# Kernel tuning notes

Measured on AMD Instinct MI355X. Metric: run time of the kernel, lower is better.

## Reference

```python
import jax, jax.numpy as jnp
import numpy as np

N_NODES = 100000
N_EDGES = 1000000
D = 64


def _sage_conv(x_src, x_self, src, dst, W_self, W_neigh, b, n_nodes):
    # mean aggregation over in-neighbors: gather src feats, segment-sum into dst
    gathered = x_src[src]                                            # [E, D]
    summed = jax.ops.segment_sum(gathered, dst, num_segments=n_nodes)  # [N, D]
    deg = jax.ops.segment_sum(jnp.ones_like(dst, dtype=x_src.dtype), dst,
                              num_segments=n_nodes)                  # [N]
    mean = summed / jnp.maximum(deg, 1.0)[:, None]  # zero-degree -> 0 (DGL semantics)
    # DGL SAGEConv: fc_self (with bias) + fc_neigh (no bias)
    return x_self @ W_self + b + mean @ W_neigh


def setup_inputs() -> dict:
    key = jax.random.key(0)
    ks = jax.random.split(key, 8)
    s = 1.0 / np.sqrt(D)
    return {
        "x": jax.random.normal(ks[0], (N_NODES, D), dtype=jnp.float32),
        "src": jax.random.randint(ks[1], (N_EDGES,), 0, N_NODES, dtype=jnp.int32),
        "dst": jax.random.randint(ks[2], (N_EDGES,), 0, N_NODES, dtype=jnp.int32),
        "W_self1": jax.random.normal(ks[3], (D, D), dtype=jnp.float32) * s,
        "W_neigh1": jax.random.normal(ks[4], (D, D), dtype=jnp.float32) * s,
        "b1": jnp.zeros((D,), dtype=jnp.float32),
        "W_self2": jax.random.normal(ks[5], (D, D), dtype=jnp.float32) * s,
        "W_neigh2": jax.random.normal(ks[6], (D, D), dtype=jnp.float32) * s,
        "b2": jnp.zeros((D,), dtype=jnp.float32),
    }


def reference(x, src, dst, W_self1, W_neigh1, b1, W_self2, W_neigh2, b2):
    n = x.shape[0]
    h = _sage_conv(x, x, src, dst, W_self1, W_neigh1, b1, n)
    h = jax.nn.relu(h)
    out = _sage_conv(h, h, src, dst, W_self2, W_neigh2, b2, n)
    return out
```

## Files before the change

kernel.cpp:

```cpp
#include <hip/hip_runtime.h>

#define DFEAT 64
typedef unsigned short bf16_t;

typedef __bf16 bf16x8 __attribute__((ext_vector_type(8)));
typedef float f32x4 __attribute__((ext_vector_type(4)));

#define NPB_SHIFT 7
#define NPB 128
#define BCAP 2048
#define ATILE 8192
#define MEAN_STRIDE 72

__device__ __forceinline__ float bf2f(unsigned short u) {
    union { unsigned int i; float f; } v;
    v.i = ((unsigned int)u) << 16;
    return v.f;
}
__device__ __forceinline__ float bflo(unsigned int u) {
    union { unsigned int i; float f; } v;
    v.i = u << 16;
    return v.f;
}
__device__ __forceinline__ float bfhi(unsigned int u) {
    union { unsigned int i; float f; } v;
    v.i = u & 0xFFFF0000u;
    return v.f;
}
__device__ __forceinline__ unsigned short f2bf(float f) {
    unsigned int u = __float_as_uint(f);
    u += 0x7FFFu + ((u >> 16) & 1u);
    return (unsigned short)(u >> 16);
}

__global__ __launch_bounds__(256) void prep_all(const int* __restrict__ src,
                                                const int* __restrict__ dst,
                                                int* __restrict__ gcur,
                                                int* __restrict__ packbuf,
                                                int n_edges, int nbuck,
                                                const float* __restrict__ x,
                                                bf16_t* __restrict__ xb, int n_half,
                                                const float* __restrict__ Ws1,
                                                const float* __restrict__ Wn1,
                                                const float* __restrict__ Ws2,
                                                const float* __restrict__ Wn2,
                                                bf16_t* __restrict__ wf1,
                                                bf16_t* __restrict__ wf2,
                                                int ab, int cb) {
    const int tid = threadIdx.x;
    const int blk = blockIdx.x;
    if (blk < ab) {
        __shared__ int hist[1024];
        __shared__ int cur[1024];
        const long ebase = (long)blk * ATILE;
        for (int i = tid; i < nbuck; i += 256) hist[i] = 0;
        __syncthreads();
        for (int i = 0; i < ATILE / 256; ++i) {
            long e = ebase + i * 256 + tid;
            if (e < n_edges) atomicAdd(&hist[dst[e] >> NPB_SHIFT], 1);
        }
        __syncthreads();
        for (int b = tid; b < nbuck; b += 256) {
            int h = hist[b];
            cur[b] = h ? atomicAdd(&gcur[b], h) : 0;
        }
        __syncthreads();
        for (int i = 0; i < ATILE / 256; ++i) {
            long e = ebase + i * 256 + tid;
            if (e < n_edges) {
                int d = dst[e];
                int b = d >> NPB_SHIFT;
                int slot = atomicAdd(&cur[b], 1);
                if (slot < BCAP)
                    packbuf[(size_t)b * BCAP + slot] = ((d & (NPB - 1)) << 17) | src[e];
            }
        }
    } else if (blk < ab + cb) {
        int t = (blk - ab) * 256 + tid;
        if (t < n_half) {
            float2 v = ((const float2*)x)[t];
            ushort2 o;
            o.x = f2bf(v.x);
            o.y = f2bf(v.y);
            ((ushort2*)xb)[t] = o;
        }
    } else {
        for (int i = tid; i < 16 * 64 * 8; i += 256) {
            int j = i & 7;
            int l = (i >> 3) & 63;
            int f = i >> 9;
            int kk = f >> 2, nt = f & 3;
            int k = kk * 32 + (l >> 4) * 8 + j;
            int col = nt * 16 + (l & 15);
            float v1 = (k < 64) ? Ws1[k * 64 + col] : Wn1[(k - 64) * 64 + col];
            float v2 = (k < 64) ? Ws2[k * 64 + col] : Wn2[(k - 64) * 64 + col];
            wf1[i] = f2bf(v1);
            wf2[i] = f2bf(v2);
        }
    }
}

__global__ __launch_bounds__(256) void fused_layer(const bf16_t* __restrict__ featb,
                                                   const int* __restrict__ gcur,
                                                   const int* __restrict__ packbuf,
                                                   const bf16_t* __restrict__ wf,
                                                   const float* __restrict__ bias,
                                                   float* __restrict__ outf,
                                                   bf16_t* __restrict__ outb,
                                                   int n_nodes, int do_relu) {
    __shared__ int    elist[BCAP];
    __shared__ bf16_t meanL[NPB * MEAN_STRIDE];
    __shared__ int    hist[NPB];
    __shared__ int    scanb[NPB];
    __shared__ int    cur[NPB];

    const int tid = threadIdx.x;
    const int b   = blockIdx.x;

    if (tid < NPB) hist[tid] = 0;
    __syncthreads();

    const int count = min(gcur[b], BCAP);
    const int* pb = packbuf + (size_t)b * BCAP;

    int pkreg[BCAP / 256];
#pragma unroll
    for (int k = 0; k < BCAP / 256; ++k) {
        int i = tid + k * 256;
        if (i < count) {
            int pk = pb[i];
            pkreg[k] = pk;
            atomicAdd(&hist[(pk >> 17) & (NPB - 1)], 1);
        }
    }
    __syncthreads();

    int hv = (tid < NPB) ? hist[tid] : 0;
    if (tid < NPB) scanb[tid] = hv;
    __syncthreads();
    for (int off = 1; off < NPB; off <<= 1) {
        int t = 0;
        if (tid < NPB && tid >= off) t = scanb[tid - off];
        __syncthreads();
        if (tid < NPB) scanb[tid] += t;
        __syncthreads();
    }
    if (tid < NPB) {
        int ex = scanb[tid] - hv;
        scanb[tid] = ex;
        cur[tid]   = ex;
    }
    __syncthreads();

#pragma unroll
    for (int k = 0; k < BCAP / 256; ++k) {
        int i = tid + k * 256;
        if (i < count) {
            int pk = pkreg[k];
            int dl = (pk >> 17) & (NPB - 1);
            int pos = atomicAdd(&cur[dl], 1);
            elist[pos] = pk & 0x1FFFF;
        }
    }
    __syncthreads();

    const int oct = tid >> 3;
    const int lo  = tid & 7;
#pragma unroll
    for (int n = 0; n < 4; ++n) {
        int r  = oct * 4 + n;
        int s0 = scanb[r];
        int c  = hist[r];
        float s0f = 0.f, s1f = 0.f, s2f = 0.f, s3f = 0.f;
        float s4f = 0.f, s5f = 0.f, s6f = 0.f, s7f = 0.f;
        int i = 0;
        for (; i + 4 <= c; i += 4) {
            int e0 = elist[s0 + i + 0];
            int e1 = elist[s0 + i + 1];
            int e2 = elist[s0 + i + 2];
            int e3 = elist[s0 + i + 3];
            uint4 u0 = *(const uint4*)(featb + (size_t)e0 * DFEAT + lo * 8);
            uint4 u1 = *(const uint4*)(featb + (size_t)e1 * DFEAT + lo * 8);
            uint4 u2 = *(const uint4*)(featb + (size_t)e2 * DFEAT + lo * 8);
            uint4 u3 = *(const uint4*)(featb + (size_t)e3 * DFEAT + lo * 8);
            s0f += bflo(u0.x) + bflo(u1.x) + bflo(u2.x) + bflo(u3.x);
            s1f += bfhi(u0.x) + bfhi(u1.x) + bfhi(u2.x) + bfhi(u3.x);
            s2f += bflo(u0.y) + bflo(u1.y) + bflo(u2.y) + bflo(u3.y);
            s3f += bfhi(u0.y) + bfhi(u1.y) + bfhi(u2.y) + bfhi(u3.y);
            s4f += bflo(u0.z) + bflo(u1.z) + bflo(u2.z) + bflo(u3.z);
            s5f += bfhi(u0.z) + bfhi(u1.z) + bfhi(u2.z) + bfhi(u3.z);
            s6f += bflo(u0.w) + bflo(u1.w) + bflo(u2.w) + bflo(u3.w);
            s7f += bfhi(u0.w) + bfhi(u1.w) + bfhi(u2.w) + bfhi(u3.w);
        }
        for (; i < c; ++i) {
            int e0 = elist[s0 + i];
            uint4 u = *(const uint4*)(featb + (size_t)e0 * DFEAT + lo * 8);
            s0f += bflo(u.x); s1f += bfhi(u.x);
            s2f += bflo(u.y); s3f += bfhi(u.y);
            s4f += bflo(u.z); s5f += bfhi(u.z);
            s6f += bflo(u.w); s7f += bfhi(u.w);
        }
        float inv = (c > 0) ? 1.0f / (float)c : 0.0f;
        uint4 o;
        o.x = (unsigned int)f2bf(s0f * inv) | ((unsigned int)f2bf(s1f * inv) << 16);
        o.y = (unsigned int)f2bf(s2f * inv) | ((unsigned int)f2bf(s3f * inv) << 16);
        o.z = (unsigned int)f2bf(s4f * inv) | ((unsigned int)f2bf(s5f * inv) << 16);
        o.w = (unsigned int)f2bf(s6f * inv) | ((unsigned int)f2bf(s7f * inv) << 16);
        *(uint4*)(meanL + (size_t)r * MEAN_STRIDE + lo * 8) = o;
    }
    __syncthreads();

    const int lane = tid & 63;
    const int wave = tid >> 6;
    const int q    = lane >> 4;
    const int cgl  = lane & 15;
    const int nodeBase = b << NPB_SHIFT;

    bf16x8 a[2][4];
#pragma unroll
    for (int slab = 0; slab < 2; ++slab) {
        const int r = wave * 32 + slab * 16 + cgl;
        int nodeA = nodeBase + r;
        if (nodeA >= n_nodes) nodeA = n_nodes - 1;
        const bf16_t* xrow = featb + (size_t)nodeA * DFEAT + q * 8;
        a[slab][0] = *(const bf16x8*)(xrow);
        a[slab][1] = *(const bf16x8*)(xrow + 32);
        const bf16_t* mrow = meanL + (size_t)r * MEAN_STRIDE + q * 8;
        a[slab][2] = *(const bf16x8*)(mrow);
        a[slab][3] = *(const bf16x8*)(mrow + 32);
    }

    f32x4 acc[2][4] = {};
#pragma unroll
    for (int nt = 0; nt < 4; ++nt) {
        bf16x8 bf[4];
#pragma unroll
        for (int kk = 0; kk < 4; ++kk)
            bf[kk] = *(const bf16x8*)(wf + (size_t)((kk * 4 + nt) * 64 + lane) * 8);
#pragma unroll
        for (int slab = 0; slab < 2; ++slab) {
#pragma unroll
            for (int kk = 0; kk < 4; ++kk)
                acc[slab][nt] = __builtin_amdgcn_mfma_f32_16x16x32_bf16(
                    a[slab][kk], bf[kk], acc[slab][nt], 0, 0, 0);
        }
    }

#pragma unroll
    for (int slab = 0; slab < 2; ++slab) {
#pragma unroll
        for (int nt = 0; nt < 4; ++nt) {
            const float bl = bias[nt * 16 + cgl];
#pragma unroll
            for (int reg = 0; reg < 4; ++reg) {
                int node = nodeBase + wave * 32 + slab * 16 + q * 4 + reg;
                if (node >= n_nodes) continue;
                float v = acc[slab][nt][reg] + bl;
                if (do_relu) v = fmaxf(v, 0.0f);
                if (outf) outf[(size_t)node * DFEAT + nt * 16 + cgl] = v;
                else      outb[(size_t)node * DFEAT + nt * 16 + cgl] = f2bf(v);
            }
        }
    }
}


extern "C" void kernel_launch(void* const* d_in, const int* in_sizes, int n_in,
                              void* d_out, int out_size, void* d_ws, size_t ws_size,
                              hipStream_t stream) {
    const float* x       = (const float*)d_in[0];
    const int*   src     = (const int*)d_in[1];
    const int*   dst     = (const int*)d_in[2];
    const float* Wself1  = (const float*)d_in[3];
    const float* Wneigh1 = (const float*)d_in[4];
    const float* b1      = (const float*)d_in[5];
    const float* Wself2  = (const float*)d_in[6];
    const float* Wneigh2 = (const float*)d_in[7];
    const float* b2      = (const float*)d_in[8];
    float* out = (float*)d_out;

    const int n_nodes = in_sizes[0] / DFEAT;
    const int n_edges = in_sizes[1];
    const int nbuck   = (n_nodes + NPB - 1) >> NPB_SHIFT;

    int* gcur       = (int*)d_ws;
    bf16_t* wf1     = (bf16_t*)(gcur + 1024);
    bf16_t* wf2     = wf1 + 16 * 64 * 8;
    int* packbuf    = (int*)(wf2 + 16 * 64 * 8);
    bf16_t* xb      = (bf16_t*)(packbuf + (size_t)nbuck * BCAP);
    bf16_t* hb      = xb + (size_t)n_nodes * DFEAT;

    const int n_half = n_nodes * DFEAT / 2;
    const int cb = (n_half + 255) / 256;
    const int ab = (n_edges + ATILE - 1) / ATILE;

    hipMemsetAsync(gcur, 0, 1024 * sizeof(int), stream);
    prep_all<<<ab + cb + 1, 256, 0, stream>>>(src, dst, gcur, packbuf, n_edges, nbuck,
                                              x, xb, n_half,
                                              Wself1, Wneigh1, Wself2, Wneigh2,
                                              wf1, wf2, ab, cb);

    fused_layer<<<nbuck, 256, 0, stream>>>(xb, gcur, packbuf, wf1, b1,
                                           nullptr, hb, n_nodes, 1);
    fused_layer<<<nbuck, 256, 0, stream>>>(hb, gcur, packbuf, wf2, b2,
                                           out, nullptr, n_nodes, 0);
}
```

Baseline: 186.7 us.

## Merge prep and both SAGE layers into one cooperative persistent kernel

Replaces the memset plus three kernel launches with a single cooperative kernel of 768 persistent blocks. Grid-wide syncs separate the cast/weight prep, edge bucketing, layer 1 and layer 2, and each block loops over buckets. Edge slices shrink from 8192 to 2048 edges, and the histogram scratch reuses the meanL shared buffer. The aim is to remove launch gaps and tail effects, at the cost of grid-sync overhead and a fixed grid that handles 782 buckets in roughly one and a bit waves. A fallback path runs the old multi-kernel scheme if the cooperative launch fails.

```diff
diff --git a/kernel.cpp b/kernel.cpp
--- a/kernel.cpp
+++ b/kernel.cpp
@@ -1,4 +1,7 @@
 #include <hip/hip_runtime.h>
+#include <hip/hip_cooperative_groups.h>
+
+namespace cg = cooperative_groups;
 
 #define DFEAT 64
 typedef unsigned short bf16_t;
@@ -9,14 +12,10 @@
 #define NPB_SHIFT 7
 #define NPB 128
 #define BCAP 2048
-#define ATILE 8192
+#define ESLICE 2048
 #define MEAN_STRIDE 72
-
-__device__ __forceinline__ float bf2f(unsigned short u) {
-    union { unsigned int i; float f; } v;
-    v.i = ((unsigned int)u) << 16;
-    return v.f;
-}
+#define COOP_GRID 768
+
 __device__ __forceinline__ float bflo(unsigned int u) {
     union { unsigned int i; float f; } v;
     v.i = u << 16;
@@ -33,96 +32,74 @@
     return (unsigned short)(u >> 16);
 }
 
-__global__ __launch_bounds__(256) void prep_all(const int* __restrict__ src,
-                                                const int* __restrict__ dst,
-                                                int* __restrict__ gcur,
-                                                int* __restrict__ packbuf,
-                                                int n_edges, int nbuck,
-                                                const float* __restrict__ x,
-                                                bf16_t* __restrict__ xb, int n_half,
-                                                const float* __restrict__ Ws1,
-                                                const float* __restrict__ Wn1,
-                                                const float* __restrict__ Ws2,
-                                                const float* __restrict__ Wn2,
-                                                bf16_t* __restrict__ wf1,
-                                                bf16_t* __restrict__ wf2,
-                                                int ab, int cb) {
+
+__device__ __forceinline__ void cast_range(const float* __restrict__ x,
+                                           bf16_t* __restrict__ xb, int lo, int hi) {
+    for (int t = lo + threadIdx.x; t < hi; t += 256) {
+        float2 v = ((const float2*)x)[t];
+        ushort2 o;
+        o.x = f2bf(v.x);
+        o.y = f2bf(v.y);
+        ((ushort2*)xb)[t] = o;
+    }
+}
+
+__device__ __forceinline__ void prep_w_dev(const float* __restrict__ Ws1,
+                                           const float* __restrict__ Wn1,
+                                           const float* __restrict__ Ws2,
+                                           const float* __restrict__ Wn2,
+                                           bf16_t* __restrict__ wf1,
+                                           bf16_t* __restrict__ wf2) {
+    for (int i = threadIdx.x; i < 16 * 64 * 8; i += 256) {
+        int j = i & 7;
+        int l = (i >> 3) & 63;
+        int f = i >> 9;
+        int kk = f >> 2, nt = f & 3;
+        int k = kk * 32 + (l >> 4) * 8 + j;
+        int col = nt * 16 + (l & 15);
+        float v1 = (k < 64) ? Ws1[k * 64 + col] : Wn1[(k - 64) * 64 + col];
+        float v2 = (k < 64) ? Ws2[k * 64 + col] : Wn2[(k - 64) * 64 + col];
+        wf1[i] = f2bf(v1);
+        wf2[i] = f2bf(v2);
+    }
+}
+
+__device__ __forceinline__ void bucket_slice(const int* __restrict__ src,
+                                             const int* __restrict__ dst,
+                                             int* __restrict__ gcur,
+                                             int* __restrict__ packbuf,
+                                             int n_edges, int nbuck, long ebase,
+                                             int* bhist, int* bcur) {
     const int tid = threadIdx.x;
-    const int blk = blockIdx.x;
-    if (blk < ab) {
-        __shared__ int hist[1024];
-        __shared__ int cur[1024];
-        const long ebase = (long)blk * ATILE;
-        for (int i = tid; i < nbuck; i += 256) hist[i] = 0;
-        __syncthreads();
-        for (int i = 0; i < ATILE / 256; ++i) {
-            long e = ebase + i * 256 + tid;
-            if (e < n_edges) atomicAdd(&hist[dst[e] >> NPB_SHIFT], 1);
-        }
-        __syncthreads();
-        for (int b = tid; b < nbuck; b += 256) {
-            int h = hist[b];
-            cur[b] = h ? atomicAdd(&gcur[b], h) : 0;
-        }
-        __syncthreads();
-        for (int i = 0; i < ATILE / 256; ++i) {
-            long e = ebase + i * 256 + tid;
-            if (e < n_edges) {
-                int d = dst[e];
-                int b = d >> NPB_SHIFT;
-                int slot = atomicAdd(&cur[b], 1);
-                if (slot < BCAP)
-                    packbuf[(size_t)b * BCAP + slot] = ((d & (NPB - 1)) << 17) | src[e];
-            }
-        }
-    } else if (blk < ab + cb) {
-        int t = (blk - ab) * 256 + tid;
-        if (t < n_half) {
-            float2 v = ((const float2*)x)[t];
-            ushort2 o;
-            o.x = f2bf(v.x);
-            o.y = f2bf(v.y);
-            ((ushort2*)xb)[t] = o;
-        }
-    } else {
-        for (int i = tid; i < 16 * 64 * 8; i += 256) {
-            int j = i & 7;
-            int l = (i >> 3) & 63;
-            int f = i >> 9;
-            int kk = f >> 2, nt = f & 3;
-            int k = kk * 32 + (l >> 4) * 8 + j;
-            int col = nt * 16 + (l & 15);
-            float v1 = (k < 64) ? Ws1[k * 64 + col] : Wn1[(k - 64) * 64 + col];
-            float v2 = (k < 64) ? Ws2[k * 64 + col] : Wn2[(k - 64) * 64 + col];
-            wf1[i] = f2bf(v1);
-            wf2[i] = f2bf(v2);
-        }
-    }
-}
-
-__global__ __launch_bounds__(256) void fused_layer(const bf16_t* __restrict__ featb,
-                                                   const int* __restrict__ gcur,
-                                                   const int* __restrict__ packbuf,
-                                                   const bf16_t* __restrict__ wf,
-                                                   const float* __restrict__ bias,
-                                                   float* __restrict__ outf,
-                                                   bf16_t* __restrict__ outb,
-                                                   int n_nodes, int do_relu) {
-    __shared__ int    elist[BCAP];
-    __shared__ bf16_t meanL[NPB * MEAN_STRIDE];
-    __shared__ int    hist[NPB];
-    __shared__ int    scanb[NPB];
-    __shared__ int    cur[NPB];
-
+    for (int i = tid; i < 1024; i += 256) bhist[i] = 0;
+    __syncthreads();
+    for (int i = 0; i < ESLICE / 256; ++i) {
+        long e = ebase + i * 256 + tid;
+        if (e < n_edges) atomicAdd(&bhist[dst[e] >> NPB_SHIFT], 1);
+    }
+    __syncthreads();
+    for (int bb = tid; bb < nbuck; bb += 256) {
+        int h = bhist[bb];
+        bcur[bb] = h ? atomicAdd(&gcur[bb], h) : 0;
+    }
+    __syncthreads();
+    for (int i = 0; i < ESLICE / 256; ++i) {
+        long e = ebase + i * 256 + tid;
+        if (e < n_edges) {
+            int d = dst[e];
+            int bb = d >> NPB_SHIFT;
+            int slot = atomicAdd(&bcur[bb], 1);
+            if (slot < BCAP)
+                packbuf[(size_t)bb * BCAP + slot] = ((d & (NPB - 1)) << 17) | src[e];
+        }
+    }
+}
+
+__device__ __forceinline__ void build_sort(const int* __restrict__ pb, int count,
+                                           int* elist, int* hist, int* scanb, int* curL) {
     const int tid = threadIdx.x;
-    const int b   = blockIdx.x;
-
     if (tid < NPB) hist[tid] = 0;
     __syncthreads();
-
-    const int count = min(gcur[b], BCAP);
-    const int* pb = packbuf + (size_t)b * BCAP;
-
     int pkreg[BCAP / 256];
 #pragma unroll
     for (int k = 0; k < BCAP / 256; ++k) {
@@ -134,7 +111,6 @@
         }
     }
     __syncthreads();
-
     int hv = (tid < NPB) ? hist[tid] : 0;
     if (tid < NPB) scanb[tid] = hv;
     __syncthreads();
@@ -148,21 +124,31 @@
     if (tid < NPB) {
         int ex = scanb[tid] - hv;
         scanb[tid] = ex;
-        cur[tid]   = ex;
-    }
-    __syncthreads();
-
+        curL[tid]  = ex;
+    }
+    __syncthreads();
 #pragma unroll
     for (int k = 0; k < BCAP / 256; ++k) {
         int i = tid + k * 256;
         if (i < count) {
             int pk = pkreg[k];
             int dl = (pk >> 17) & (NPB - 1);
-            int pos = atomicAdd(&cur[dl], 1);
+            int pos = atomicAdd(&curL[dl], 1);
             elist[pos] = pk & 0x1FFFF;
         }
     }
     __syncthreads();
+}
+
+__device__ __forceinline__ void layer_body(const bf16_t* __restrict__ featb,
+                                           const bf16_t* __restrict__ wf,
+                                           const float* __restrict__ bias,
+                                           float* __restrict__ outf,
+                                           bf16_t* __restrict__ outb,
+                                           int n_nodes, int do_relu, int b,
+                                           int* elist, bf16_t* meanL,
+                                           int* hist, int* scanb) {
+    const int tid = threadIdx.x;
 
     const int oct = tid >> 3;
     const int lo  = tid & 7;
@@ -264,6 +250,114 @@
     }
 }
 
+__global__ __launch_bounds__(256, 3) void sage_all(
+        const int* __restrict__ src, const int* __restrict__ dst,
+        const float* __restrict__ x,
+        const float* __restrict__ Ws1, const float* __restrict__ Wn1,
+        const float* __restrict__ bias1,
+        const float* __restrict__ Ws2, const float* __restrict__ Wn2,
+        const float* __restrict__ bias2,
+        float* __restrict__ out,
+        int* __restrict__ gcur, bf16_t* __restrict__ wf1, bf16_t* __restrict__ wf2,
+        int* __restrict__ packbuf, bf16_t* __restrict__ xb, bf16_t* __restrict__ hb,
+        int n_nodes, int n_edges, int n_half, int nbuck) {
+    __shared__ int    elist[BCAP];
+    __shared__ bf16_t meanL[NPB * MEAN_STRIDE];
+    __shared__ int    hist[NPB];
+    __shared__ int    scanb[NPB];
+    __shared__ int    curL[NPB];
+
+    cg::grid_group grid = cg::this_grid();
+    const int tid  = threadIdx.x;
+    const int blk  = blockIdx.x;
+    const int nblk = gridDim.x;
+
+    if (blk == 0)
+        for (int i = tid; i < 1024; i += 256) gcur[i] = 0;
+    {
+        int per = (n_half + nblk - 1) / nblk;
+        int lo  = blk * per;
+        int hi  = min(lo + per, n_half);
+        cast_range(x, xb, lo, hi);
+    }
+    if (blk == nblk - 1)
+        prep_w_dev(Ws1, Wn1, Ws2, Wn2, wf1, wf2);
+    grid.sync();
+
+    {
+        int eblk = (n_edges + ESLICE - 1) / ESLICE;
+        if (blk < eblk)
+            bucket_slice(src, dst, gcur, packbuf, n_edges, nbuck,
+                         (long)blk * ESLICE, (int*)meanL, ((int*)meanL) + 1024);
+    }
+    grid.sync();
+
+    for (int b = blk; b < nbuck; b += nblk) {
+        build_sort(packbuf + (size_t)b * BCAP, min(gcur[b], BCAP),
+                   elist, hist, scanb, curL);
+        layer_body(xb, wf1, bias1, nullptr, hb, n_nodes, 1, b,
+                   elist, meanL, hist, scanb);
+        __syncthreads();
+    }
+    grid.sync();
+
+    for (int b = blk; b < nbuck; b += nblk) {
+        build_sort(packbuf + (size_t)b * BCAP, min(gcur[b], BCAP),
+                   elist, hist, scanb, curL);
+        layer_body(hb, wf2, bias2, out, nullptr, n_nodes, 0, b,
+                   elist, meanL, hist, scanb);
+        __syncthreads();
+    }
+}
+
+__global__ __launch_bounds__(256) void prep_all_fb(const int* __restrict__ src,
+                                                   const int* __restrict__ dst,
+                                                   int* __restrict__ gcur,
+                                                   int* __restrict__ packbuf,
+                                                   int n_edges, int nbuck,
+                                                   const float* __restrict__ x,
+                                                   bf16_t* __restrict__ xb, int n_half,
+                                                   const float* __restrict__ Ws1,
+                                                   const float* __restrict__ Wn1,
+                                                   const float* __restrict__ Ws2,
+                                                   const float* __restrict__ Wn2,
+                                                   bf16_t* __restrict__ wf1,
+                                                   bf16_t* __restrict__ wf2,
+                                                   int ab, int cb) {
+    __shared__ int bhist[1024];
+    __shared__ int bcur[1024];
+    const int blk = blockIdx.x;
+    if (blk < ab) {
+        bucket_slice(src, dst, gcur, packbuf, n_edges, nbuck,
+                     (long)blk * ESLICE, bhist, bcur);
+    } else if (blk < ab + cb) {
+        int lo = (blk - ab) * 256;
+        cast_range(x, xb, lo, min(lo + 256, n_half));
+    } else {
+        prep_w_dev(Ws1, Wn1, Ws2, Wn2, wf1, wf2);
+    }
+}
+
+__global__ __launch_bounds__(256) void fused_layer_fb(const bf16_t* __restrict__ featb,
+                                                      const int* __restrict__ gcur,
+                                                      const int* __restrict__ packbuf,
+                                                      const bf16_t* __restrict__ wf,
+                                                      const float* __restrict__ bias,
+                                                      float* __restrict__ outf,
+                                                      bf16_t* __restrict__ outb,
+                                                      int n_nodes, int do_relu) {
+    __shared__ int    elist[BCAP];
+    __shared__ bf16_t meanL[NPB * MEAN_STRIDE];
+    __shared__ int    hist[NPB];
+    __shared__ int    scanb[NPB];
+    __shared__ int    curL[NPB];
+    const int b = blockIdx.x;
+    build_sort(packbuf + (size_t)b * BCAP, min(gcur[b], BCAP),
+               elist, hist, scanb, curL);
+    layer_body(featb, wf, bias, outf, outb, n_nodes, do_relu, b,
+               elist, meanL, hist, scanb);
+}
+
 
 extern "C" void kernel_launch(void* const* d_in, const int* in_sizes, int n_in,
                               void* d_out, int out_size, void* d_ws, size_t ws_size,
@@ -279,9 +373,10 @@
     const float* b2      = (const float*)d_in[8];
     float* out = (float*)d_out;
 
-    const int n_nodes = in_sizes[0] / DFEAT;
-    const int n_edges = in_sizes[1];
-    const int nbuck   = (n_nodes + NPB - 1) >> NPB_SHIFT;
+    int n_nodes = in_sizes[0] / DFEAT;
+    int n_edges = in_sizes[1];
+    int nbuck   = (n_nodes + NPB - 1) >> NPB_SHIFT;
+    int n_half  = n_nodes * DFEAT / 2;
 
     int* gcur       = (int*)d_ws;
     bf16_t* wf1     = (bf16_t*)(gcur + 1024);
@@ -290,18 +385,26 @@
     bf16_t* xb      = (bf16_t*)(packbuf + (size_t)nbuck * BCAP);
     bf16_t* hb      = xb + (size_t)n_nodes * DFEAT;
 
-    const int n_half = n_nodes * DFEAT / 2;
-    const int cb = (n_half + 255) / 256;
-    const int ab = (n_edges + ATILE - 1) / ATILE;
-
-    hipMemsetAsync(gcur, 0, 1024 * sizeof(int), stream);
-    prep_all<<<ab + cb + 1, 256, 0, stream>>>(src, dst, gcur, packbuf, n_edges, nbuck,
-                                              x, xb, n_half,
-                                              Wself1, Wneigh1, Wself2, Wneigh2,
-                                              wf1, wf2, ab, cb);
-
-    fused_layer<<<nbuck, 256, 0, stream>>>(xb, gcur, packbuf, wf1, b1,
-                                           nullptr, hb, n_nodes, 1);
-    fused_layer<<<nbuck, 256, 0, stream>>>(hb, gcur, packbuf, wf2, b2,
-                                           out, nullptr, n_nodes, 0);
-}
+    void* args[] = {
+        &src, &dst, &x, &Wself1, &Wneigh1, &b1, &Wself2, &Wneigh2, &b2, &out,
+        &gcur, &wf1, &wf2, &packbuf, &xb, &hb,
+        &n_nodes, &n_edges, &n_half, &nbuck
+    };
+    hipError_t err = hipLaunchCooperativeKernel((const void*)sage_all,
+                                                dim3(COOP_GRID), dim3(256),
+                                                args, 0, stream);
+    if (err != hipSuccess) {
+        (void)hipGetLastError();
+        int ab = (n_edges + ESLICE - 1) / ESLICE;
+        int cb = (n_half + 255) / 256;
+        hipMemsetAsync(gcur, 0, 1024 * sizeof(int), stream);
+        prep_all_fb<<<ab + cb + 1, 256, 0, stream>>>(src, dst, gcur, packbuf,
+                                                     n_edges, nbuck, x, xb, n_half,
+                                                     Wself1, Wneigh1, Wself2, Wneigh2,
+                                                     wf1, wf2, ab, cb);
+        fused_layer_fb<<<nbuck, 256, 0, stream>>>(xb, gcur, packbuf, wf1, b1,
+                                                  nullptr, hb, n_nodes, 1);
+        fused_layer_fb<<<nbuck, 256, 0, stream>>>(hb, gcur, packbuf, wf2, b2,
+                                                  out, nullptr, n_nodes, 0);
+    }
+}
```

Result: slower. 499.9 us (+167.8%).
